# Kernel tuning notes

Hardware: AMD Instinct MI355X
Metric: run time of the kernel (lower is better)

## Reference

```python
import jax, jax.numpy as jnp
import numpy as np

BH, BW = 4, 4  # bin_size_h, bin_size_w
BN_EPS = 1e-5


def _patch_split(t, bh, bw):
    # b c (bh ph) (bw pw) -> b (bh bw) (ph pw) c
    b, c, h, w = t.shape
    ph, pw = h // bh, w // bw
    t = t.reshape(b, c, bh, ph, bw, pw).transpose(0, 2, 4, 3, 5, 1)
    return t.reshape(b, bh * bw, ph * pw, c)


def _patch_recover(t, bh, bw, ph, pw):
    # b (bh bw) (ph pw) c -> b c (bh ph) (bw pw)
    b, n, p, c = t.shape
    t = t.reshape(b, bh, bw, ph, pw, c).transpose(0, 5, 1, 3, 2, 4)
    return t.reshape(b, c, bh * ph, bw * pw)


def setup_inputs() -> dict:
    key = jax.random.key(0)
    ks = jax.random.split(key, 16)
    b, C, h, w = 4, 512, 128, 128      # proj_dim = 512
    mid = C // 2                        # 256
    CM = 19 * 4                         # num_classes * num_local_prototype = 76
    return {
        "x": jax.random.normal(ks[0], (b, C, h, w), jnp.float32),
        "sim_mat": jax.random.normal(ks[1], (b, CM, h, w), jnp.float32),
        "global_cls_centers": jax.random.normal(ks[2], (19, 4, C), jnp.float32),
        "Wq": jax.random.normal(ks[3], (C, mid), jnp.float32) * 0.02,
        "bq": jax.random.normal(ks[4], (mid,), jnp.float32) * 0.02,
        "Wk": jax.random.normal(ks[5], (C, mid), jnp.float32) * 0.02,
        "bk": jax.random.normal(ks[6], (mid,), jnp.float32) * 0.02,
        "Wv": jax.random.normal(ks[7], (C, mid), jnp.float32) * 0.02,
        "bv": jax.random.normal(ks[8], (mid,), jnp.float32) * 0.02,
        "Wc": jax.random.normal(ks[9], (mid, C), jnp.float32) * 0.02,
        "bn_gamma": jax.random.uniform(ks[10], (C,), jnp.float32, 0.5, 1.5),
        "bn_beta": jax.random.normal(ks[11], (C,), jnp.float32) * 0.1,
        "bn_mean": jax.random.normal(ks[12], (C,), jnp.float32) * 0.1,
        "bn_var": jax.random.uniform(ks[13], (C,), jnp.float32, 0.5, 1.5),
    }


def reference(x, sim_mat, global_cls_centers, Wq, bq, Wk, bk, Wv, bv, Wc,
              bn_gamma, bn_beta, bn_mean, bn_var):
    b, C, h, w = x.shape
    CM = sim_mat.shape[1]
    ph, pw = h // BH, w // BW

    # pool_cam: adaptive avg pool to (BH, BW) == per-patch mean
    patch_cls_score = sim_mat.reshape(b, CM, BH, ph, BW, pw).mean(axis=(3, 5))  # [b,CM,BH,BW]

    sm = _patch_split(sim_mat, BH, BW)   # [b, N, P, CM]
    xs = _patch_split(x, BH, BW)         # [b, N, P, C]

    # patch_confidence: [b, N, CM, 1]
    conf = patch_cls_score.reshape(b, CM, BH * BW).transpose(0, 2, 1)[..., None]

    sm = jax.nn.softmax(sm, axis=2)      # softmax over pixels within patch
    local = jnp.einsum('bnpc,bnpk->bnck', sm, xs) * conf  # [b, N, CM, C]

    g = global_cls_centers.reshape(CM, C)  # (c m) k

    q = xs @ Wq + bq        # [b, N, P, mid]
    k = local @ Wk + bk     # [b, N, CM, mid]
    v = g @ Wv + bv         # [CM, mid] (identical across b, n -> broadcast)

    att = jax.nn.softmax(jnp.einsum('bnpm,bncm->bnpc', q, k), axis=-1)
    out = jnp.einsum('bnpc,cm->bnpm', att, v)               # [b, N, P, mid]

    out = _patch_recover(out, BH, BW, ph, pw)               # [b, mid, h, w]

    # conv_out: 1x1 conv (no bias) + BN (eval) + ReLU
    y = jnp.einsum('bmhw,mk->bkhw', out, Wc)
    inv = bn_gamma / jnp.sqrt(bn_var + BN_EPS)
    y = y * inv[None, :, None, None] + (bn_beta - bn_mean * inv)[None, :, None, None]
    y = jax.nn.relu(y)
    return (y, patch_cls_score)
```

## Files before the change

### kernel.cpp

```cpp
#include <hip/hip_runtime.h>

#define CM_    76
#define CMP_   80

typedef __attribute__((ext_vector_type(4))) float f32x4;
typedef __attribute__((ext_vector_type(8))) short bf16x8;

__device__ __forceinline__ unsigned short f2bf(float f) {
  union { float f; unsigned u; } v; v.f = f;
  unsigned r = v.u + 0x7FFFu + ((v.u >> 16) & 1u);
  return (unsigned short)(r >> 16);
}
__device__ __forceinline__ unsigned pack2(float a, float b) {
  return (unsigned)f2bf(a) | ((unsigned)f2bf(b) << 16);
}
__device__ __forceinline__ float bf2f(unsigned short u) {
  union { unsigned u; float f; } v; v.u = ((unsigned)u) << 16; return v.f;
}

#define OFF_ROWMAX  0
#define OFF_SCALE   4864
#define OFF_BK2     9728
#define OFF_INV     14848
#define OFF_ADD     15360
#define OFF_WKBQ    15872
#define OFF_BQKADD  16384
#define OFF_CBB     16896
#define OFF_LOCALBF 16900
#define OFF_WQKT    1327620
#define OFF_VWT     2638340
#define OFF_WQWKT   2662916
#define OFF_WVWCT   2793988

__global__ __launch_bounds__(256) void kW_pre(
    const float* __restrict__ Wq, const float* __restrict__ Wk,
    const float* __restrict__ Wv, const float* __restrict__ Wc,
    unsigned short* __restrict__ WqWkT, unsigned short* __restrict__ WvWcT) {
  const int r0 = (blockIdx.x >> 3) * 64, c0 = (blockIdx.x & 7) * 64;
  const int sel = blockIdx.y;
  __shared__ __align__(16) unsigned short Asm[64 * 40];
  __shared__ __align__(16) unsigned short Bsm[64 * 40];
  const int t = threadIdx.x, lane = t & 63, w = t >> 6;
  const int lo = lane & 15, hi = lane >> 4;
  f32x4 acc[4];
#pragma unroll
  for (int cT = 0; cT < 4; ++cT) acc[cT] = (f32x4){0.f, 0.f, 0.f, 0.f};
  const float* Bsrc = sel ? Wv : Wk;
  for (int kc = 0; kc < 8; ++kc) {
    const int k0 = kc * 32;
    __syncthreads();
    {
      int n = t >> 2, mq = (t & 3) * 8;
      const float* src = Bsrc + (size_t)(c0 + n) * 256 + k0 + mq;
      float4 v0 = *(const float4*)src, v1 = *(const float4*)(src + 4);
      unsigned* d = (unsigned*)&Bsm[n * 40 + mq];
      d[0] = pack2(v0.x, v0.y); d[1] = pack2(v0.z, v0.w);
      d[2] = pack2(v1.x, v1.y); d[3] = pack2(v1.z, v1.w);
    }
    if (sel == 0) {
      int r = t >> 2, mq = (t & 3) * 8;
      const float* src = Wq + (size_t)(r0 + r) * 256 + k0 + mq;
      float4 v0 = *(const float4*)src, v1 = *(const float4*)(src + 4);
      unsigned* d = (unsigned*)&Asm[r * 40 + mq];
      d[0] = pack2(v0.x, v0.y); d[1] = pack2(v0.z, v0.w);
      d[2] = pack2(v1.x, v1.y); d[3] = pack2(v1.z, v1.w);
    } else {
      int m = t >> 3, c2q = (t & 7) * 8;
      const float* src = Wc + (size_t)(k0 + m) * 512 + r0 + c2q;
      float4 v0 = *(const float4*)src, v1 = *(const float4*)(src + 4);
      Asm[(c2q + 0) * 40 + m] = f2bf(v0.x); Asm[(c2q + 1) * 40 + m] = f2bf(v0.y);
      Asm[(c2q + 2) * 40 + m] = f2bf(v0.z); Asm[(c2q + 3) * 40 + m] = f2bf(v0.w);
      Asm[(c2q + 4) * 40 + m] = f2bf(v1.x); Asm[(c2q + 5) * 40 + m] = f2bf(v1.y);
      Asm[(c2q + 6) * 40 + m] = f2bf(v1.z); Asm[(c2q + 7) * 40 + m] = f2bf(v1.w);
    }
    __syncthreads();
    bf16x8 afr = *(bf16x8*)(&Asm[(w * 16 + lo) * 40 + hi * 8]);
#pragma unroll
    for (int cT = 0; cT < 4; ++cT) {
      bf16x8 bfr = *(bf16x8*)(&Bsm[(cT * 16 + lo) * 40 + hi * 8]);
      acc[cT] = __builtin_amdgcn_mfma_f32_16x16x32_bf16(afr, bfr, acc[cT], 0, 0, 0);
    }
  }
  unsigned short* dst = sel ? WvWcT : WqWkT;
#pragma unroll
  for (int cT = 0; cT < 4; ++cT)
#pragma unroll
    for (int rr = 0; rr < 4; ++rr)
      dst[(size_t)(r0 + w * 16 + hi * 4 + rr) * 512 + c0 + cT * 16 + lo] = f2bf(acc[cT][rr]);
}

__global__ __launch_bounds__(256) void kB_pre(
    const float* __restrict__ Wk, const float* __restrict__ Wq,
    const float* __restrict__ bq, const float* __restrict__ bk,
    const float* __restrict__ gamma, const float* __restrict__ beta,
    const float* __restrict__ mean, const float* __restrict__ var,
    float* __restrict__ wkbq, float* __restrict__ bqkadd,
    float* __restrict__ invp, float* __restrict__ addp, float* __restrict__ cbbp) {
  const int c = blockIdx.x * 256 + threadIdx.x;
  const float* wkr = Wk + (size_t)c * 256;
  const float* wqr = Wq + (size_t)c * 256;
  float s1 = 0.f, s2 = 0.f;
  for (int m = 0; m < 256; ++m) { s1 += wkr[m] * bq[m]; s2 += wqr[m] * bk[m]; }
  wkbq[c] = s1; bqkadd[c] = s2;
  float iv = gamma[c] * rsqrtf(var[c] + 1e-5f);
  invp[c] = iv; addp[c] = beta[c] - mean[c] * iv;
  if (c == 0) {
    float s = 0.f;
    for (int m = 0; m < 256; ++m) s += bq[m] * bk[m];
    cbbp[0] = s;
  }
}

__global__ __launch_bounds__(256) void k1_stats(
    const float* __restrict__ sim, float* __restrict__ pcs,
    float* __restrict__ rowmax, float* __restrict__ scale_arr) {
  const int cm = blockIdx.x, inst = blockIdx.y;
  const int b = inst >> 4, n = inst & 15, bh = n >> 2, bw = n & 3;
  const float* base = sim + ((size_t)(b * CM_ + cm) << 14);
  const int t = threadIdx.x;
  float v[4];
  float lsum = 0.f, lmax = -1e30f;
#pragma unroll
  for (int i = 0; i < 4; ++i) {
    int p = t + (i << 8);
    int pix = ((bh * 32 + (p >> 5)) << 7) + bw * 32 + (p & 31);
    float xv = base[pix];
    v[i] = xv; lsum += xv; lmax = fmaxf(lmax, xv);
  }
#pragma unroll
  for (int off = 32; off; off >>= 1) {
    lsum += __shfl_down(lsum, off);
    lmax = fmaxf(lmax, __shfl_down(lmax, off));
  }
  __shared__ float ssum[4], smax[4], bc[2];
  const int wid = t >> 6;
  if ((t & 63) == 0) { ssum[wid] = lsum; smax[wid] = lmax; }
  __syncthreads();
  if (t == 0) {
    bc[0] = ssum[0] + ssum[1] + ssum[2] + ssum[3];
    bc[1] = fmaxf(fmaxf(smax[0], smax[1]), fmaxf(smax[2], smax[3]));
  }
  __syncthreads();
  const float M = bc[1];
  float le = 0.f;
#pragma unroll
  for (int i = 0; i < 4; ++i) le += __expf(v[i] - M);
#pragma unroll
  for (int off = 32; off; off >>= 1) le += __shfl_down(le, off);
  if ((t & 63) == 0) ssum[wid] = le;
  __syncthreads();
  if (t == 0) {
    float E = ssum[0] + ssum[1] + ssum[2] + ssum[3];
    float conf = bc[0] * (1.f / 1024.f);
    pcs[((b * CM_ + cm) << 4) + n] = conf;
    rowmax[inst * CM_ + cm] = M;
    scale_arr[inst * CM_ + cm] = conf / E;
  }
}

__global__ __launch_bounds__(256) void k2_local(
    const float* __restrict__ x, const float* __restrict__ sim,
    const float* __restrict__ rowmax, const float* __restrict__ scale_arr,
    unsigned short* __restrict__ local_bf) {
  const int cc = blockIdx.x, inst = blockIdx.y;
  const int b = inst >> 4, n = inst & 15, bh = n >> 2, bw = n & 3;
  __shared__ unsigned short As[CMP_ * 136];
  const int t = threadIdx.x, lane = t & 63, w = t >> 6;
  const int lo = lane & 15, hi = lane >> 4;
  const int chw = cc * 64 + w * 16;
  const int cm0 = t >> 3, pq = t & 7;

  f32x4 acc[5];
#pragma unroll
  for (int T = 0; T < 5; ++T) acc[T] = (f32x4){0.f, 0.f, 0.f, 0.f};

  for (int pc = 0; pc < 8; ++pc) {
    __syncthreads();
#pragma unroll
    for (int j = 0; j < 3; ++j) {
      int cm = cm0 + 32 * j;
      if (cm < CMP_) {
        if (cm < CM_) {
          float rm = rowmax[inst * CM_ + cm];
          float sc = scale_arr[inst * CM_ + cm];
          const float* srow = sim + ((size_t)(b * CM_ + cm) << 14);
#pragma unroll
          for (int i = 0; i < 4; ++i) {
            int pxl = i * 32 + pq * 4;
            int gpx = pc * 128 + pxl;
            int pix = ((bh * 32 + (gpx >> 5)) << 7) + bw * 32 + (gpx & 31);
            float4 vv = *(const float4*)(srow + pix);
            unsigned l32 = pack2(sc * __expf(vv.x - rm), sc * __expf(vv.y - rm));
            unsigned h32 = pack2(sc * __expf(vv.z - rm), sc * __expf(vv.w - rm));
            *(unsigned long long*)(&As[cm * 136 + pxl]) =
                (unsigned long long)l32 | ((unsigned long long)h32 << 32);
          }
        } else {
#pragma unroll
          for (int i = 0; i < 4; ++i)
            *(unsigned long long*)(&As[cm * 136 + i * 32 + pq * 4]) = 0ull;
        }
      }
    }
    __syncthreads();
#pragma unroll
    for (int ks = 0; ks < 4; ++ks) {
      int gpx0 = pc * 128 + ks * 32 + hi * 8;
      int pix0 = ((bh * 32 + (gpx0 >> 5)) << 7) + bw * 32 + (gpx0 & 31);
      const float* xr = x + (((size_t)(b * 512 + chw + lo)) << 14) + pix0;
      float4 v0 = *(const float4*)(xr);
      float4 v1 = *(const float4*)(xr + 4);
      bf16x8 bfr;
      ((unsigned*)&bfr)[0] = pack2(v0.x, v0.y);
      ((unsigned*)&bfr)[1] = pack2(v0.z, v0.w);
      ((unsigned*)&bfr)[2] = pack2(v1.x, v1.y);
      ((unsigned*)&bfr)[3] = pack2(v1.z, v1.w);
#pragma unroll
      for (int T = 0; T < 5; ++T) {
        bf16x8 afr = *(bf16x8*)(&As[(T * 16 + lo) * 136 + ks * 32 + hi * 8]);
        acc[T] = __builtin_amdgcn_mfma_f32_16x16x32_bf16(afr, bfr, acc[T], 0, 0, 0);
      }
    }
  }
#pragma unroll
  for (int T = 0; T < 5; ++T)
#pragma unroll
    for (int r = 0; r < 4; ++r) {
      int cm = T * 16 + hi * 4 + r;
      if (cm < CM_)
        local_bf[((size_t)inst * CMP_ + cm) * 512 + chw + lo] = f2bf(acc[T][r]);
    }
}

__global__ __launch_bounds__(256) void kbk(
    const unsigned short* __restrict__ local_bf, const float* __restrict__ wkbq,
    const float* __restrict__ cbbp, float* __restrict__ bk2) {
  const int inst = blockIdx.x, t = threadIdx.x;
  __shared__ float wsm[512];
  for (int i = t; i < 512; i += 256) wsm[i] = wkbq[i];
  __syncthreads();
  const float cbb = cbbp[0];
  const int q = t & 3;
#pragma unroll
  for (int base = 0; base < 128; base += 64) {
    int idx = base + (t >> 2);
    if (idx < CM_) {
      const unsigned short* row = local_bf + ((size_t)inst * CMP_ + idx) * 512 + q * 128;
      float s = 0.f;
      for (int j = 0; j < 128; j += 2) {
        unsigned u = *(const unsigned*)(row + j);
        s += bf2f((unsigned short)(u & 0xFFFF)) * wsm[q * 128 + j]
           + bf2f((unsigned short)(u >> 16)) * wsm[q * 128 + j + 1];
      }
      s += __shfl_down(s, 2);
      s += __shfl_down(s, 1);
      if (q == 0) bk2[inst * CMP_ + idx] = s + cbb;
    } else if (idx < CMP_ && q == 0) {
      bk2[inst * CMP_ + idx] = -1e30f;
    }
  }
}

__global__ __launch_bounds__(256) void k3n_wqkt(
    const unsigned short* __restrict__ local_bf, const unsigned short* __restrict__ WqWkT,
    const float* __restrict__ bqkadd, unsigned short* __restrict__ Wqkt) {
  const int blkc = blockIdx.x, inst = blockIdx.y;
  const int t = threadIdx.x, lane = t & 63, w = t >> 6;
  const int lo = lane & 15, hi = lane >> 4;
  const int cbase = blkc * 128 + w * 32;
  f32x4 acc[5][2];
#pragma unroll
  for (int cT = 0; cT < 2; ++cT) {
    float bv_ = bqkadd[cbase + cT * 16 + lo];
#pragma unroll
    for (int T = 0; T < 5; ++T) acc[T][cT] = (f32x4){bv_, bv_, bv_, bv_};
  }
  const unsigned short* Abase = local_bf + (size_t)inst * 40960;
#pragma unroll 4
  for (int ks = 0; ks < 16; ++ks) {
    const int k = ks * 32 + hi * 8;
    bf16x8 af[5];
#pragma unroll
    for (int T = 0; T < 5; ++T)
      af[T] = *(const bf16x8*)(Abase + (size_t)(T * 16 + lo) * 512 + k);
#pragma unroll
    for (int cT = 0; cT < 2; ++cT) {
      bf16x8 bfr = *(const bf16x8*)(WqWkT + (size_t)(cbase + cT * 16 + lo) * 512 + k);
#pragma unroll
      for (int T = 0; T < 5; ++T)
        acc[T][cT] = __builtin_amdgcn_mfma_f32_16x16x32_bf16(af[T], bfr, acc[T][cT], 0, 0, 0);
    }
  }
#pragma unroll
  for (int T = 0; T < 5; ++T)
#pragma unroll
    for (int cT = 0; cT < 2; ++cT)
#pragma unroll
      for (int r = 0; r < 4; ++r) {
        int cm = T * 16 + hi * 4 + r;
        Wqkt[(size_t)inst * 40960 + (size_t)cm * 512 + cbase + cT * 16 + lo] =
            f2bf(acc[T][cT][r]);
      }
}

__global__ __launch_bounds__(256) void kV_vwt(
    const unsigned short* __restrict__ WvWcT, const float* __restrict__ g,
    const float* __restrict__ bv, const float* __restrict__ Wc,
    unsigned short* __restrict__ vWt) {
  const int blk = blockIdx.x, half = blockIdx.y;
  const int t = threadIdx.x, lane = t & 63, w = t >> 6;
  const int lo = lane & 15, hi = lane >> 4;
  __shared__ float bvp[4][64];
  __shared__ float bvs[64];
  {
    int c2l = t & 63, part = t >> 6;
    float s = 0.f;
    for (int m = part * 64; m < part * 64 + 64; ++m)
      s += bv[m] * Wc[(size_t)m * 512 + blk * 64 + c2l];
    bvp[part][c2l] = s;
  }
  __syncthreads();
  if (t < 64) bvs[t] = bvp[0][t] + bvp[1][t] + bvp[2][t] + bvp[3][t];
  __syncthreads();
  const int r2 = blk * 64 + w * 16;
  f32x4 acc[3];
#pragma unroll
  for (int j = 0; j < 3; ++j) acc[j] = (f32x4){0.f, 0.f, 0.f, 0.f};
#pragma unroll 4
  for (int ks = 0; ks < 16; ++ks) {
    const int k = ks * 32 + hi * 8;
    bf16x8 afr = *(const bf16x8*)(WvWcT + (size_t)(r2 + lo) * 512 + k);
#pragma unroll
    for (int j = 0; j < 3; ++j) {
      int cm = (half * 3 + j) * 16 + lo;
      cm = cm > 75 ? 75 : cm;
      const float* gr = g + (size_t)cm * 512 + k;
      float4 v0 = *(const float4*)gr, v1 = *(const float4*)(gr + 4);
      bf16x8 bfr;
      ((unsigned*)&bfr)[0] = pack2(v0.x, v0.y);
      ((unsigned*)&bfr)[1] = pack2(v0.z, v0.w);
      ((unsigned*)&bfr)[2] = pack2(v1.x, v1.y);
      ((unsigned*)&bfr)[3] = pack2(v1.z, v1.w);
      acc[j] = __builtin_amdgcn_mfma_f32_16x16x32_bf16(afr, bfr, acc[j], 0, 0, 0);
    }
  }
#pragma unroll
  for (int j = 0; j < 3; ++j)
#pragma unroll
    for (int rr = 0; rr < 4; ++rr) {
      int c2g = blk * 64 + w * 16 + hi * 4 + rr;
      vWt[(size_t)c2g * 96 + (half * 3 + j) * 16 + lo] =
          f2bf(acc[j][rr] + bvs[w * 16 + hi * 4 + rr]);
    }
}

__global__ __launch_bounds__(256) void k4_attn(
    const float* __restrict__ x, const unsigned short* __restrict__ Wqkt,
    const float* __restrict__ bk2, const unsigned short* __restrict__ vWt,
    const float* __restrict__ inv_arr, const float* __restrict__ add_arr,
    float* __restrict__ y) {
  const int pt = blockIdx.x, inst = blockIdx.y;
  const int b = inst >> 4, n = inst & 15, bh = n >> 2, bw = n & 3;
  __shared__ unsigned short Xs[4][32 * 72];
  __shared__ unsigned short Att[4][32 * 96];
  __shared__ float bn_s[1024];
  const int t = threadIdx.x, lane = t & 63, w = t >> 6;
  const int lo = lane & 15, hi = lane >> 4;
  const int pq = lane & 7, chp0 = lane >> 3;

  for (int i = t; i < 512; i += 256) { bn_s[i] = inv_arr[i]; bn_s[512 + i] = add_arr[i]; }

  const int imgrow = bh * 32 + pt * 4 + w;
  const size_t pixbase = (size_t)imgrow * 128 + bw * 32;
  const size_t xrowbase = (((size_t)b * 512) << 14) + pixbase;
  const unsigned short* Wi = Wqkt + (size_t)inst * 40960;

  f32x4 acc[2][5];
#pragma unroll
  for (int T = 0; T < 5; ++T) {
    f32x4 bv;
#pragma unroll
    for (int r = 0; r < 4; ++r) bv[r] = bk2[inst * CMP_ + T * 16 + hi * 4 + r];
    acc[0][T] = bv; acc[1][T] = bv;
  }

  for (int kc = 0; kc < 8; ++kc) {
#pragma unroll
    for (int i = 0; i < 4; ++i) {
      int chp = chp0 + i * 8;
      int ch = kc * 64 + chp * 2;
      const float* xa = x + xrowbase + ((size_t)ch << 14) + pq * 4;
      float4 va = *(const float4*)(xa);
      float4 vb = *(const float4*)(xa + 16384);
      unsigned short* dst = &Xs[w][(pq * 4) * 72 + chp * 2];
      *(unsigned*)(dst + 0 * 72) = pack2(va.x, vb.x);
      *(unsigned*)(dst + 1 * 72) = pack2(va.y, vb.y);
      *(unsigned*)(dst + 2 * 72) = pack2(va.z, vb.z);
      *(unsigned*)(dst + 3 * 72) = pack2(va.w, vb.w);
    }
#pragma unroll
    for (int ks = 0; ks < 2; ++ks) {
      int kb = kc * 64 + ks * 32 + hi * 8;
      bf16x8 b0 = *(bf16x8*)(&Xs[w][lo * 72 + ks * 32 + hi * 8]);
      bf16x8 b1 = *(bf16x8*)(&Xs[w][(16 + lo) * 72 + ks * 32 + hi * 8]);
#pragma unroll
      for (int T = 0; T < 5; ++T) {
        bf16x8 afr = *(const bf16x8*)(Wi + (size_t)(T * 16 + lo) * 512 + kb);
        acc[0][T] = __builtin_amdgcn_mfma_f32_16x16x32_bf16(afr, b0, acc[0][T], 0, 0, 0);
        acc[1][T] = __builtin_amdgcn_mfma_f32_16x16x32_bf16(afr, b1, acc[1][T], 0, 0, 0);
      }
    }
  }

#pragma unroll
  for (int p = 0; p < 2; ++p) {
    float m = -1e30f;
#pragma unroll
    for (int T = 0; T < 5; ++T)
#pragma unroll
      for (int r = 0; r < 4; ++r) m = fmaxf(m, acc[p][T][r]);
    m = fmaxf(m, __shfl_xor(m, 16));
    m = fmaxf(m, __shfl_xor(m, 32));
    float e[5][4];
    float s = 0.f;
#pragma unroll
    for (int T = 0; T < 5; ++T)
#pragma unroll
      for (int r = 0; r < 4; ++r) { float ev = __expf(acc[p][T][r] - m); e[T][r] = ev; s += ev; }
    s += __shfl_xor(s, 16);
    s += __shfl_xor(s, 32);
    float rinv = 1.f / s;
    int px = p * 16 + lo;
#pragma unroll
    for (int T = 0; T < 5; ++T) {
      unsigned l32 = pack2(e[T][0] * rinv, e[T][1] * rinv);
      unsigned h32 = pack2(e[T][2] * rinv, e[T][3] * rinv);
      *(unsigned long long*)(&Att[w][px * 96 + T * 16 + hi * 4]) =
          (unsigned long long)l32 | ((unsigned long long)h32 << 32);
    }
    *(unsigned long long*)(&Att[w][px * 96 + 80 + hi * 4]) = 0ull;
  }

  __syncthreads();

  bf16x8 bfr3[2][3];
#pragma unroll
  for (int p = 0; p < 2; ++p)
#pragma unroll
    for (int ks = 0; ks < 3; ++ks)
      bfr3[p][ks] = *(bf16x8*)(&Att[w][(p * 16 + lo) * 96 + ks * 32 + hi * 8]);

  for (int cT = 0; cT < 32; ++cT) {
    f32x4 a0 = (f32x4){0.f, 0.f, 0.f, 0.f}, a1 = a0;
    const unsigned short* vr = vWt + (size_t)(cT * 16 + lo) * 96;
#pragma unroll
    for (int ks = 0; ks < 3; ++ks) {
      bf16x8 afr = *(const bf16x8*)(vr + ks * 32 + hi * 8);
      a0 = __builtin_amdgcn_mfma_f32_16x16x32_bf16(afr, bfr3[0][ks], a0, 0, 0, 0);
      a1 = __builtin_amdgcn_mfma_f32_16x16x32_bf16(afr, bfr3[1][ks], a1, 0, 0, 0);
    }
    f32x4 inv4 = *(f32x4*)(&bn_s[cT * 16 + hi * 4]);
    f32x4 add4 = *(f32x4*)(&bn_s[512 + cT * 16 + hi * 4]);
#pragma unroll
    for (int r = 0; r < 4; ++r) {
      int ch = cT * 16 + hi * 4 + r;
      float v0 = fmaxf(a0[r] * inv4[r] + add4[r], 0.f);
      float v1 = fmaxf(a1[r] * inv4[r] + add4[r], 0.f);
      size_t yb = (((size_t)(b * 512 + ch)) << 14) + pixbase;
      y[yb + lo] = v0;
      y[yb + 16 + lo] = v1;
    }
  }
}

extern "C" void kernel_launch(void* const* d_in, const int* in_sizes, int n_in,
                              void* d_out, int out_size, void* d_ws, size_t ws_size,
                              hipStream_t stream) {
  (void)in_sizes; (void)n_in; (void)out_size; (void)ws_size;
  const float* x     = (const float*)d_in[0];
  const float* sim   = (const float*)d_in[1];
  const float* g     = (const float*)d_in[2];
  const float* Wq    = (const float*)d_in[3];
  const float* bq    = (const float*)d_in[4];
  const float* Wk    = (const float*)d_in[5];
  const float* bk    = (const float*)d_in[6];
  const float* Wv    = (const float*)d_in[7];
  const float* bv    = (const float*)d_in[8];
  const float* Wc    = (const float*)d_in[9];
  const float* gamma = (const float*)d_in[10];
  const float* beta  = (const float*)d_in[11];
  const float* mean  = (const float*)d_in[12];
  const float* var   = (const float*)d_in[13];
  float* out = (float*)d_out;
  float* ws  = (float*)d_ws;
  float* y   = out;
  float* pcs = out + 33554432;
  unsigned short* localbf = (unsigned short*)(ws + OFF_LOCALBF);
  unsigned short* Wqkt    = (unsigned short*)(ws + OFF_WQKT);
  unsigned short* vWt     = (unsigned short*)(ws + OFF_VWT);
  unsigned short* WqWkT   = (unsigned short*)(ws + OFF_WQWKT);
  unsigned short* WvWcT   = (unsigned short*)(ws + OFF_WVWCT);

  hipLaunchKernelGGL(kW_pre, dim3(64, 2), dim3(256), 0, stream,
                     Wq, Wk, Wv, Wc, WqWkT, WvWcT);
  hipLaunchKernelGGL(kB_pre, dim3(2), dim3(256), 0, stream,
                     Wk, Wq, bq, bk, gamma, beta, mean, var,
                     ws + OFF_WKBQ, ws + OFF_BQKADD, ws + OFF_INV, ws + OFF_ADD,
                     ws + OFF_CBB);
  hipLaunchKernelGGL(k1_stats, dim3(CM_, 64), dim3(256), 0, stream,
                     sim, pcs, ws + OFF_ROWMAX, ws + OFF_SCALE);
  hipLaunchKernelGGL(k2_local, dim3(8, 64), dim3(256), 0, stream,
                     x, sim, ws + OFF_ROWMAX, ws + OFF_SCALE, localbf);
  hipLaunchKernelGGL(kbk, dim3(64), dim3(256), 0, stream,
                     localbf, ws + OFF_WKBQ, ws + OFF_CBB, ws + OFF_BK2);
  hipLaunchKernelGGL(k3n_wqkt, dim3(4, 64), dim3(256), 0, stream,
                     localbf, WqWkT, ws + OFF_BQKADD, Wqkt);
  hipLaunchKernelGGL(kV_vwt, dim3(8, 2), dim3(256), 0, stream,
                     WvWcT, g, bv, Wc, vWt);
  hipLaunchKernelGGL(k4_attn, dim3(8, 64), dim3(256), 0, stream,
                     x, Wqkt, ws + OFF_BK2, vWt,
                     ws + OFF_INV, ws + OFF_ADD, y);
}
```

Baseline: 430.8 us.

## Precompute bf16 exp-softmax weights in stats kernel and fuse bias-key reduction into local

The stats kernel now writes scaled softmax weights as bf16 into a patch-major workspace buffer. The local-feature kernel then reads them directly as the MFMA A operand instead of re-reading sim and recomputing exp in each of 8 channel blocks. The separate bias-key kernel is folded into the local kernel's epilogue as a shuffle reduction plus atomicAdd. The weight-bias precompute kernel is merged into kW_pre as an extra block column. Costs: an extra ~5MB bf16 write/read, A-fragment loads straight from global without LDS, and a float atomic summation order that is no longer deterministic.

```diff
diff --git a/kernel.cpp b/kernel.cpp
--- a/kernel.cpp
+++ b/kernel.cpp
@@ -14,30 +14,47 @@
 __device__ __forceinline__ unsigned pack2(float a, float b) {
   return (unsigned)f2bf(a) | ((unsigned)f2bf(b) << 16);
 }
-__device__ __forceinline__ float bf2f(unsigned short u) {
-  union { unsigned u; float f; } v; v.u = ((unsigned)u) << 16; return v.f;
-}
-
-#define OFF_ROWMAX  0
-#define OFF_SCALE   4864
-#define OFF_BK2     9728
-#define OFF_INV     14848
-#define OFF_ADD     15360
-#define OFF_WKBQ    15872
-#define OFF_BQKADD  16384
-#define OFF_CBB     16896
-#define OFF_LOCALBF 16900
-#define OFF_WQKT    1327620
-#define OFF_VWT     2638340
-#define OFF_WQWKT   2662916
-#define OFF_WVWCT   2793988
+
+#define OFF_BK2     0
+#define OFF_INV     5120
+#define OFF_ADD     5632
+#define OFF_WKBQ    6144
+#define OFF_BQKADD  6656
+#define OFF_CBB     7168
+#define OFF_EXPSIM  7172
+#define OFF_LOCALBF 2628612
+#define OFF_WQKT    3939332
+#define OFF_VWT     5250052
+#define OFF_WQWKT   5274628
+#define OFF_WVWCT   5405700
 
 __global__ __launch_bounds__(256) void kW_pre(
     const float* __restrict__ Wq, const float* __restrict__ Wk,
     const float* __restrict__ Wv, const float* __restrict__ Wc,
-    unsigned short* __restrict__ WqWkT, unsigned short* __restrict__ WvWcT) {
+    const float* __restrict__ bq, const float* __restrict__ bk,
+    const float* __restrict__ gamma, const float* __restrict__ beta,
+    const float* __restrict__ mean, const float* __restrict__ var,
+    unsigned short* __restrict__ WqWkT, unsigned short* __restrict__ WvWcT,
+    float* __restrict__ wkbq, float* __restrict__ bqkadd,
+    float* __restrict__ invp, float* __restrict__ addp, float* __restrict__ cbbp) {
+  const int sel = blockIdx.y;
+  if (blockIdx.x == 64) {
+    const int c = sel * 256 + threadIdx.x;
+    const float* wkr = Wk + (size_t)c * 256;
+    const float* wqr = Wq + (size_t)c * 256;
+    float s1 = 0.f, s2 = 0.f;
+    for (int m = 0; m < 256; ++m) { s1 += wkr[m] * bq[m]; s2 += wqr[m] * bk[m]; }
+    wkbq[c] = s1; bqkadd[c] = s2;
+    float iv = gamma[c] * rsqrtf(var[c] + 1e-5f);
+    invp[c] = iv; addp[c] = beta[c] - mean[c] * iv;
+    if (c == 0) {
+      float s = 0.f;
+      for (int m = 0; m < 256; ++m) s += bq[m] * bk[m];
+      cbbp[0] = s;
+    }
+    return;
+  }
   const int r0 = (blockIdx.x >> 3) * 64, c0 = (blockIdx.x & 7) * 64;
-  const int sel = blockIdx.y;
   __shared__ __align__(16) unsigned short Asm[64 * 40];
   __shared__ __align__(16) unsigned short Bsm[64 * 40];
   const int t = threadIdx.x, lane = t & 63, w = t >> 6;
@@ -50,10 +67,10 @@
     const int k0 = kc * 32;
     __syncthreads();
     {
-      int n = t >> 2, mq = (t & 3) * 8;
-      const float* src = Bsrc + (size_t)(c0 + n) * 256 + k0 + mq;
+      int nn = t >> 2, mq = (t & 3) * 8;
+      const float* src = Bsrc + (size_t)(c0 + nn) * 256 + k0 + mq;
       float4 v0 = *(const float4*)src, v1 = *(const float4*)(src + 4);
-      unsigned* d = (unsigned*)&Bsm[n * 40 + mq];
+      unsigned* d = (unsigned*)&Bsm[nn * 40 + mq];
       d[0] = pack2(v0.x, v0.y); d[1] = pack2(v0.z, v0.w);
       d[2] = pack2(v1.x, v1.y); d[3] = pack2(v1.z, v1.w);
     }
@@ -89,35 +106,20 @@
       dst[(size_t)(r0 + w * 16 + hi * 4 + rr) * 512 + c0 + cT * 16 + lo] = f2bf(acc[cT][rr]);
 }
 
-__global__ __launch_bounds__(256) void kB_pre(
-    const float* __restrict__ Wk, const float* __restrict__ Wq,
-    const float* __restrict__ bq, const float* __restrict__ bk,
-    const float* __restrict__ gamma, const float* __restrict__ beta,
-    const float* __restrict__ mean, const float* __restrict__ var,
-    float* __restrict__ wkbq, float* __restrict__ bqkadd,
-    float* __restrict__ invp, float* __restrict__ addp, float* __restrict__ cbbp) {
-  const int c = blockIdx.x * 256 + threadIdx.x;
-  const float* wkr = Wk + (size_t)c * 256;
-  const float* wqr = Wq + (size_t)c * 256;
-  float s1 = 0.f, s2 = 0.f;
-  for (int m = 0; m < 256; ++m) { s1 += wkr[m] * bq[m]; s2 += wqr[m] * bk[m]; }
-  wkbq[c] = s1; bqkadd[c] = s2;
-  float iv = gamma[c] * rsqrtf(var[c] + 1e-5f);
-  invp[c] = iv; addp[c] = beta[c] - mean[c] * iv;
-  if (c == 0) {
-    float s = 0.f;
-    for (int m = 0; m < 256; ++m) s += bq[m] * bk[m];
-    cbbp[0] = s;
-  }
-}
-
 __global__ __launch_bounds__(256) void k1_stats(
     const float* __restrict__ sim, float* __restrict__ pcs,
-    float* __restrict__ rowmax, float* __restrict__ scale_arr) {
+    const float* __restrict__ cbbp,
+    unsigned short* __restrict__ expsim, float* __restrict__ bk2) {
   const int cm = blockIdx.x, inst = blockIdx.y;
+  const int t = threadIdx.x;
+  unsigned short* erow = expsim + (size_t)inst * 81920 + (size_t)cm * 1024;
+  if (cm >= CM_) {
+    ((unsigned long long*)erow)[t] = 0ull;
+    if (t == 0) bk2[inst * CMP_ + cm] = -1e30f;
+    return;
+  }
   const int b = inst >> 4, n = inst & 15, bh = n >> 2, bw = n & 3;
   const float* base = sim + ((size_t)(b * CM_ + cm) << 14);
-  const int t = threadIdx.x;
   float v[4];
   float lsum = 0.f, lmax = -1e30f;
 #pragma unroll
@@ -153,112 +155,63 @@
     float E = ssum[0] + ssum[1] + ssum[2] + ssum[3];
     float conf = bc[0] * (1.f / 1024.f);
     pcs[((b * CM_ + cm) << 4) + n] = conf;
-    rowmax[inst * CM_ + cm] = M;
-    scale_arr[inst * CM_ + cm] = conf / E;
+    bk2[inst * CMP_ + cm] = cbbp[0];
+    bc[0] = conf / E;
+  }
+  __syncthreads();
+  const float sc = bc[0];
+#pragma unroll
+  for (int i = 0; i < 4; ++i) {
+    int p = t + (i << 8);
+    erow[p] = f2bf(sc * __expf(v[i] - M));
   }
 }
 
 __global__ __launch_bounds__(256) void k2_local(
-    const float* __restrict__ x, const float* __restrict__ sim,
-    const float* __restrict__ rowmax, const float* __restrict__ scale_arr,
-    unsigned short* __restrict__ local_bf) {
+    const float* __restrict__ x, const unsigned short* __restrict__ expsim,
+    const float* __restrict__ wkbq,
+    unsigned short* __restrict__ local_bf, float* __restrict__ bk2) {
   const int cc = blockIdx.x, inst = blockIdx.y;
   const int b = inst >> 4, n = inst & 15, bh = n >> 2, bw = n & 3;
-  __shared__ unsigned short As[CMP_ * 136];
   const int t = threadIdx.x, lane = t & 63, w = t >> 6;
   const int lo = lane & 15, hi = lane >> 4;
   const int chw = cc * 64 + w * 16;
-  const int cm0 = t >> 3, pq = t & 7;
-
+  const unsigned short* Abase = expsim + (size_t)inst * 81920;
+  const float* xch = x + (((size_t)(b * 512 + chw + lo)) << 14) + bw * 32 + hi * 8;
+  const int rowb = bh * 32;
   f32x4 acc[5];
 #pragma unroll
   for (int T = 0; T < 5; ++T) acc[T] = (f32x4){0.f, 0.f, 0.f, 0.f};
-
-  for (int pc = 0; pc < 8; ++pc) {
-    __syncthreads();
-#pragma unroll
-    for (int j = 0; j < 3; ++j) {
-      int cm = cm0 + 32 * j;
-      if (cm < CMP_) {
-        if (cm < CM_) {
-          float rm = rowmax[inst * CM_ + cm];
-          float sc = scale_arr[inst * CM_ + cm];
-          const float* srow = sim + ((size_t)(b * CM_ + cm) << 14);
-#pragma unroll
-          for (int i = 0; i < 4; ++i) {
-            int pxl = i * 32 + pq * 4;
-            int gpx = pc * 128 + pxl;
-            int pix = ((bh * 32 + (gpx >> 5)) << 7) + bw * 32 + (gpx & 31);
-            float4 vv = *(const float4*)(srow + pix);
-            unsigned l32 = pack2(sc * __expf(vv.x - rm), sc * __expf(vv.y - rm));
-            unsigned h32 = pack2(sc * __expf(vv.z - rm), sc * __expf(vv.w - rm));
-            *(unsigned long long*)(&As[cm * 136 + pxl]) =
-                (unsigned long long)l32 | ((unsigned long long)h32 << 32);
-          }
-        } else {
-#pragma unroll
-          for (int i = 0; i < 4; ++i)
-            *(unsigned long long*)(&As[cm * 136 + i * 32 + pq * 4]) = 0ull;
-        }
-      }
-    }
-    __syncthreads();
-#pragma unroll
-    for (int ks = 0; ks < 4; ++ks) {
-      int gpx0 = pc * 128 + ks * 32 + hi * 8;
-      int pix0 = ((bh * 32 + (gpx0 >> 5)) << 7) + bw * 32 + (gpx0 & 31);
-      const float* xr = x + (((size_t)(b * 512 + chw + lo)) << 14) + pix0;
-      float4 v0 = *(const float4*)(xr);
-      float4 v1 = *(const float4*)(xr + 4);
-      bf16x8 bfr;
-      ((unsigned*)&bfr)[0] = pack2(v0.x, v0.y);
-      ((unsigned*)&bfr)[1] = pack2(v0.z, v0.w);
-      ((unsigned*)&bfr)[2] = pack2(v1.x, v1.y);
-      ((unsigned*)&bfr)[3] = pack2(v1.z, v1.w);
-#pragma unroll
-      for (int T = 0; T < 5; ++T) {
-        bf16x8 afr = *(bf16x8*)(&As[(T * 16 + lo) * 136 + ks * 32 + hi * 8]);
-        acc[T] = __builtin_amdgcn_mfma_f32_16x16x32_bf16(afr, bfr, acc[T], 0, 0, 0);
-      }
-    }
-  }
+#pragma unroll 4
+  for (int ks = 0; ks < 32; ++ks) {
+    const int k = ks * 32 + hi * 8;
+    const float* xr = xch + ((size_t)(rowb + ks) << 7);
+    float4 v0 = *(const float4*)(xr);
+    float4 v1 = *(const float4*)(xr + 4);
+    bf16x8 bfr;
+    ((unsigned*)&bfr)[0] = pack2(v0.x, v0.y);
+    ((unsigned*)&bfr)[1] = pack2(v0.z, v0.w);
+    ((unsigned*)&bfr)[2] = pack2(v1.x, v1.y);
+    ((unsigned*)&bfr)[3] = pack2(v1.z, v1.w);
+#pragma unroll
+    for (int T = 0; T < 5; ++T) {
+      bf16x8 afr = *(const bf16x8*)(Abase + (size_t)(T * 16 + lo) * 1024 + k);
+      acc[T] = __builtin_amdgcn_mfma_f32_16x16x32_bf16(afr, bfr, acc[T], 0, 0, 0);
+    }
+  }
+  const float wk = wkbq[chw + lo];
 #pragma unroll
   for (int T = 0; T < 5; ++T)
 #pragma unroll
     for (int r = 0; r < 4; ++r) {
       int cm = T * 16 + hi * 4 + r;
-      if (cm < CM_)
-        local_bf[((size_t)inst * CMP_ + cm) * 512 + chw + lo] = f2bf(acc[T][r]);
-    }
-}
-
-__global__ __launch_bounds__(256) void kbk(
-    const unsigned short* __restrict__ local_bf, const float* __restrict__ wkbq,
-    const float* __restrict__ cbbp, float* __restrict__ bk2) {
-  const int inst = blockIdx.x, t = threadIdx.x;
-  __shared__ float wsm[512];
-  for (int i = t; i < 512; i += 256) wsm[i] = wkbq[i];
-  __syncthreads();
-  const float cbb = cbbp[0];
-  const int q = t & 3;
-#pragma unroll
-  for (int base = 0; base < 128; base += 64) {
-    int idx = base + (t >> 2);
-    if (idx < CM_) {
-      const unsigned short* row = local_bf + ((size_t)inst * CMP_ + idx) * 512 + q * 128;
-      float s = 0.f;
-      for (int j = 0; j < 128; j += 2) {
-        unsigned u = *(const unsigned*)(row + j);
-        s += bf2f((unsigned short)(u & 0xFFFF)) * wsm[q * 128 + j]
-           + bf2f((unsigned short)(u >> 16)) * wsm[q * 128 + j + 1];
-      }
-      s += __shfl_down(s, 2);
-      s += __shfl_down(s, 1);
-      if (q == 0) bk2[inst * CMP_ + idx] = s + cbb;
-    } else if (idx < CMP_ && q == 0) {
-      bk2[inst * CMP_ + idx] = -1e30f;
-    }
-  }
+      float av = acc[T][r];
+      local_bf[((size_t)inst * CMP_ + cm) * 512 + chw + lo] = f2bf(av);
+      float p = av * wk;
+      p += __shfl_xor(p, 1); p += __shfl_xor(p, 2);
+      p += __shfl_xor(p, 4); p += __shfl_xor(p, 8);
+      if (lo == 0 && cm < CM_) atomicAdd(&bk2[inst * CMP_ + cm], p);
+    }
 }
 
 __global__ __launch_bounds__(256) void k3n_wqkt(
@@ -495,24 +448,21 @@
   float* ws  = (float*)d_ws;
   float* y   = out;
   float* pcs = out + 33554432;
+  unsigned short* expsim  = (unsigned short*)(ws + OFF_EXPSIM);
   unsigned short* localbf = (unsigned short*)(ws + OFF_LOCALBF);
   unsigned short* Wqkt    = (unsigned short*)(ws + OFF_WQKT);
   unsigned short* vWt     = (unsigned short*)(ws + OFF_VWT);
   unsigned short* WqWkT   = (unsigned short*)(ws + OFF_WQWKT);
   unsigned short* WvWcT   = (unsigned short*)(ws + OFF_WVWCT);
 
-  hipLaunchKernelGGL(kW_pre, dim3(64, 2), dim3(256), 0, stream,
-                     Wq, Wk, Wv, Wc, WqWkT, WvWcT);
-  hipLaunchKernelGGL(kB_pre, dim3(2), dim3(256), 0, stream,
-                     Wk, Wq, bq, bk, gamma, beta, mean, var,
-                     ws + OFF_WKBQ, ws + OFF_BQKADD, ws + OFF_INV, ws + OFF_ADD,
-                     ws + OFF_CBB);
-  hipLaunchKernelGGL(k1_stats, dim3(CM_, 64), dim3(256), 0, stream,
-                     sim, pcs, ws + OFF_ROWMAX, ws + OFF_SCALE);
+  hipLaunchKernelGGL(kW_pre, dim3(65, 2), dim3(256), 0, stream,
+                     Wq, Wk, Wv, Wc, bq, bk, gamma, beta, mean, var,
+                     WqWkT, WvWcT, ws + OFF_WKBQ, ws + OFF_BQKADD,
+                     ws + OFF_INV, ws + OFF_ADD, ws + OFF_CBB);
+  hipLaunchKernelGGL(k1_stats, dim3(CMP_, 64), dim3(256), 0, stream,
+                     sim, pcs, ws + OFF_CBB, expsim, ws + OFF_BK2);
   hipLaunchKernelGGL(k2_local, dim3(8, 64), dim3(256), 0, stream,
-                     x, sim, ws + OFF_ROWMAX, ws + OFF_SCALE, localbf);
-  hipLaunchKernelGGL(kbk, dim3(64), dim3(256), 0, stream,
-                     localbf, ws + OFF_WKBQ, ws + OFF_CBB, ws + OFF_BK2);
+                     x, expsim, ws + OFF_WKBQ, localbf, ws + OFF_BK2);
   hipLaunchKernelGGL(k3n_wqkt, dim3(4, 64), dim3(256), 0, stream,
                      localbf, WqWkT, ws + OFF_BQKADD, Wqkt);
   hipLaunchKernelGGL(kV_vwt, dim3(8, 2), dim3(256), 0, stream,
```

After: 424.8 us. Within noise of the previous version (-1.4%).
